# Optimization experiments

Measured on AMD Instinct MI355X. Metric: run time of the kernel, lower is better.

The kernel has to match this reference:

```python
import jax, jax.numpy as jnp
import numpy as np

EPS = 1e-5

def _lin(x, w, b):
    return x @ w + b

def _ln(x, scale, bias):
    m = jnp.mean(x, axis=-1, keepdims=True)
    v = jnp.var(x, axis=-1, keepdims=True)
    return (x - m) / jnp.sqrt(v + EPS) * scale + bias

def setup_inputs() -> dict:
    key = jax.random.key(0)
    B, N, F, OUT, TRI = 4, 128, 128, 128, 8
    ks = iter(jax.random.split(key, 64))
    def lin_params(fan_in, fan_out):
        s = 1.0 / np.sqrt(fan_in)
        w = jax.random.uniform(next(ks), (fan_in, fan_out), minval=-s, maxval=s, dtype=jnp.float32)
        b = jax.random.uniform(next(ks), (fan_out,), minval=-s, maxval=s, dtype=jnp.float32)
        return w, b
    inp = {}
    inp['node_fts'] = jax.random.normal(next(ks), (B, N, F), dtype=jnp.float32)
    inp['edge_fts'] = jax.random.normal(next(ks), (B, N, N, F), dtype=jnp.float32)
    inp['graph_fts'] = jax.random.normal(next(ks), (B, F), dtype=jnp.float32)
    inp['hidden'] = jax.random.normal(next(ks), (B, N, F), dtype=jnp.float32)
    inp['adj_matrix'] = jax.random.randint(next(ks), (B, N, N), 0, 2, dtype=jnp.int32)
    inp['m1_w'], inp['m1_b'] = lin_params(2 * F, OUT)
    inp['m2_w'], inp['m2_b'] = lin_params(2 * F, OUT)
    inp['me_w'], inp['me_b'] = lin_params(F, OUT)
    inp['mg_w'], inp['mg_b'] = lin_params(F, OUT)
    inp['mlp1_w'], inp['mlp1_b'] = lin_params(OUT, OUT)
    inp['mlp2_w'], inp['mlp2_b'] = lin_params(OUT, OUT)
    inp['o1_w'], inp['o1_b'] = lin_params(2 * F, OUT)
    inp['o2_w'], inp['o2_b'] = lin_params(OUT, OUT)
    inp['t1_w'], inp['t1_b'] = lin_params(2 * F, TRI)
    inp['t2_w'], inp['t2_b'] = lin_params(2 * F, TRI)
    inp['te1_w'], inp['te1_b'] = lin_params(F, TRI)
    inp['te2_w'], inp['te2_b'] = lin_params(F, TRI)
    inp['te3_w'], inp['te3_b'] = lin_params(F, TRI)
    inp['tg_w'], inp['tg_b'] = lin_params(F, TRI)
    inp['o3_w'], inp['o3_b'] = lin_params(TRI, OUT)
    inp['norm_scale'] = jnp.ones((OUT,), dtype=jnp.float32)
    inp['norm_bias'] = jnp.zeros((OUT,), dtype=jnp.float32)
    return inp

def reference(node_fts, edge_fts, graph_fts, hidden, adj_matrix,
              m1_w, m1_b, m2_w, m2_b, me_w, me_b, mg_w, mg_b,
              mlp1_w, mlp1_b, mlp2_w, mlp2_b,
              o1_w, o1_b, o2_w, o2_b,
              t1_w, t1_b, t2_w, t2_b,
              te1_w, te1_b, te2_w, te2_b, te3_w, te3_b,
              tg_w, tg_b, o3_w, o3_b, norm_scale, norm_bias):
    z = jnp.concatenate([node_fts, hidden], axis=-1)          # [B,N,2F]
    msg_1 = _lin(z, m1_w, m1_b)                                # [B,N,H]
    msg_2 = _lin(z, m2_w, m2_b)
    msg_e = _lin(edge_fts, me_w, me_b)                         # [B,N,N,H]
    msg_g = _lin(graph_fts, mg_w, mg_b)                        # [B,H]
    msgs = msg_1[:, None, :, :] + msg_2[:, :, None, :] + msg_e + msg_g[:, None, None, :]
    # msg_mlp: ReLU -> Linear -> ReLU -> Linear
    msgs = _lin(jax.nn.relu(_lin(jax.nn.relu(msgs), mlp1_w, mlp1_b)), mlp2_w, mlp2_b)
    # triplet messages (note: original code reuses t_1 for tri_3 -- faithful)
    tri_1 = _lin(z, t1_w, t1_b)                                # [B,N,T]
    tri_2 = _lin(z, t2_w, t2_b)
    tri_3 = _lin(z, t1_w, t1_b)
    tri_e_1 = _lin(edge_fts, te1_w, te1_b)                     # [B,N,N,T]
    tri_e_2 = _lin(edge_fts, te2_w, te2_b)
    tri_e_3 = _lin(edge_fts, te3_w, te3_b)
    tri_g = _lin(graph_fts, tg_w, tg_b)                        # [B,T]
    triplets = (tri_1[:, :, None, None, :] + tri_2[:, None, :, None, :]
                + tri_3[:, None, None, :, :]
                + tri_e_1[:, :, :, None, :] + tri_e_2[:, :, None, :, :]
                + tri_e_3[:, None, :, :, :]
                + tri_g[:, None, None, None, :])               # [B,N,N,N,T]
    tri_msgs = _lin(jnp.max(triplets, axis=1), o3_w, o3_b)     # [B,N,N,OUT]
    tri_msgs = _ln(jax.nn.relu(tri_msgs), norm_scale, norm_bias)
    # masked max aggregation
    maxarg = jnp.where(adj_matrix[..., None] == 1, msgs, -1e9)
    msgs_agg = jnp.max(maxarg, axis=1)                         # [B,N,H]
    out = jax.nn.relu(_lin(z, o1_w, o1_b) + _lin(msgs_agg, o2_w, o2_b))
    out = _ln(out, norm_scale, norm_bias)
    return out, tri_msgs
```

## Files before the change

### kernel.cpp

```cpp
#include <hip/hip_runtime.h>
#include <hip/hip_bf16.h>
#include <cstddef>
#include <cstdint>

typedef __attribute__((ext_vector_type(8))) short bf16x8;
typedef __attribute__((ext_vector_type(4))) float f32x4;
typedef unsigned short ushort_t;

__device__ __forceinline__ ushort_t f2b(float f) {
    uint32_t x = __float_as_uint(f);
    uint32_t r = (x + 0x7FFFu + ((x >> 16) & 1u)) >> 16;
    return (ushort_t)r;
}
__device__ __forceinline__ float b2f(ushort_t u) {
    return __uint_as_float(((uint32_t)u) << 16);
}

__global__ void prep_kernel(const float* __restrict__ m1_w, const float* __restrict__ m2_w,
                            const float* __restrict__ o1_w, const float* __restrict__ t1_w,
                            const float* __restrict__ t2_w,
                            const float* __restrict__ me_w, const float* __restrict__ mlp1_w,
                            const float* __restrict__ mlp2_w,
                            const float* __restrict__ te1_w, const float* __restrict__ te2_w,
                            const float* __restrict__ te3_w,
                            const float* __restrict__ graph_fts,
                            const float* __restrict__ mg_w, const float* __restrict__ mg_b,
                            const float* __restrict__ m1_b,
                            const float* __restrict__ tg_w, const float* __restrict__ t2_b,
                            const float* __restrict__ tg_b,
                            ushort_t* __restrict__ Wnt,
                            ushort_t* __restrict__ Wme, ushort_t* __restrict__ Wm1,
                            ushort_t* __restrict__ Wm2, ushort_t* __restrict__ TEt,
                            float* __restrict__ G1, float* __restrict__ TG) {
    int idx = blockIdx.x * 256 + threadIdx.x;
    if (idx < 106496) {
        int o = idx >> 8, k = idx & 255;
        float v = 0.0f;
        if (o < 128)       v = m1_w[k * 128 + o];
        else if (o < 256)  v = m2_w[k * 128 + (o - 128)];
        else if (o < 384)  v = o1_w[k * 128 + (o - 256)];
        else if (o < 392)  v = t1_w[k * 8 + (o - 384)];
        else if (o < 400)  v = t2_w[k * 8 + (o - 392)];
        Wnt[idx] = f2b(v);
    } else if (idx < 122880) {
        int t = idx - 106496, o = t >> 7, h = t & 127;
        Wme[t] = f2b(me_w[h * 128 + o]);
    } else if (idx < 139264) {
        int t = idx - 122880, o = t >> 7, h = t & 127;
        Wm1[t] = f2b(mlp1_w[h * 128 + o]);
    } else if (idx < 155648) {
        int t = idx - 139264, o = t >> 7, h = t & 127;
        Wm2[t] = f2b(mlp2_w[h * 128 + o]);
    } else if (idx < 159744) {
        int t = idx - 155648, c = t >> 7, h = t & 127;
        float v = 0.0f;
        if (c < 8)       v = te1_w[h * 8 + c];
        else if (c < 16) v = te2_w[h * 8 + (c - 8)];
        else if (c < 24) v = te3_w[h * 8 + (c - 16)];
        TEt[t] = f2b(v);
    } else if (idx < 160256) {
        int t = idx - 159744, b = t >> 7, h = t & 127;
        float a = m1_b[h] + mg_b[h];
        #pragma unroll 4
        for (int k = 0; k < 128; k++) a = fmaf(graph_fts[b * 128 + k], mg_w[k * 128 + h], a);
        G1[t] = a;
    } else if (idx < 160288) {
        int t = idx - 160256, b = t >> 3, tt = t & 7;
        float a = t2_b[tt] + tg_b[tt];
        #pragma unroll 4
        for (int k = 0; k < 128; k++) a = fmaf(graph_fts[b * 128 + k], tg_w[k * 8 + tt], a);
        TG[t] = a;
    }
}

__global__ __launch_bounds__(256)
void node_gemm(const float* __restrict__ node_fts, const float* __restrict__ hidden,
               const ushort_t* __restrict__ Wnt,
               const float* __restrict__ G1, const float* __restrict__ m2_b,
               const float* __restrict__ o1_b, const float* __restrict__ t1_b,
               const float* __restrict__ TG,
               float* __restrict__ M1, float* __restrict__ M2, float* __restrict__ O1z,
               float* __restrict__ T1v, float* __restrict__ TT2) {
    __shared__ ushort_t Zs[32 * 256];
    char* Zb = (char*)Zs;
    const int tid = threadIdx.x;
    const int blk = blockIdx.x;
    const int b = blk >> 2, q = blk & 3;
    const int row0 = b * 128 + q * 32;
    const int w = tid >> 6, l = tid & 63, g = l >> 4, lq = l & 15;

    const float4* nsrc = reinterpret_cast<const float4*>(node_fts + (size_t)row0 * 128);
    const float4* hsrc = reinterpret_cast<const float4*>(hidden + (size_t)row0 * 128);
    #pragma unroll
    for (int p = 0; p < 8; p++) {
        int idx = tid + p * 256;
        int r = idx >> 6, c4 = idx & 63;
        float4 v = (c4 < 32) ? nsrc[r * 32 + c4] : hsrc[r * 32 + (c4 - 32)];
        uint2 pk;
        pk.x = (uint32_t)f2b(v.x) | ((uint32_t)f2b(v.y) << 16);
        pk.y = (uint32_t)f2b(v.z) | ((uint32_t)f2b(v.w) << 16);
        *reinterpret_cast<uint2*>(Zb + r * 512 + (((c4 >> 1) ^ (r & 7)) << 4) + (c4 & 1) * 8) = pk;
    }
    __syncthreads();

    for (int mt = w; mt < 26; mt += 4) {
        f32x4 acc0 = (f32x4){0.f, 0.f, 0.f, 0.f};
        f32x4 acc1 = (f32x4){0.f, 0.f, 0.f, 0.f};
        const ushort_t* arow = Wnt + (size_t)(mt * 16 + lq) * 256;
        #pragma unroll
        for (int ks = 0; ks < 8; ks++) {
            bf16x8 a = *reinterpret_cast<const bf16x8*>(arow + ks * 32 + g * 8);
            int j0 = lq, j1 = 16 + lq;
            bf16x8 b0 = *reinterpret_cast<const bf16x8*>(Zb + j0 * 512 + (((ks * 4 + g) ^ (j0 & 7)) << 4));
            bf16x8 b1 = *reinterpret_cast<const bf16x8*>(Zb + j1 * 512 + (((ks * 4 + g) ^ (j1 & 7)) << 4));
            acc0 = __builtin_amdgcn_mfma_f32_16x16x32_bf16(a, b0, acc0, 0, 0, 0);
            acc1 = __builtin_amdgcn_mfma_f32_16x16x32_bf16(a, b1, acc1, 0, 0, 0);
        }
        #pragma unroll
        for (int half = 0; half < 2; half++) {
            const f32x4 acc = half ? acc1 : acc0;
            const int grow = row0 + half * 16 + lq;
            #pragma unroll
            for (int c = 0; c < 4; c++) {
                int o = mt * 16 + g * 4 + c;
                float v = acc[c];
                if (o < 128)       M1[(size_t)grow * 128 + o] = v + G1[b * 128 + o];
                else if (o < 256)  M2[(size_t)grow * 128 + (o - 128)] = v + m2_b[o - 128];
                else if (o < 384)  O1z[(size_t)grow * 128 + (o - 256)] = v + o1_b[o - 256];
                else if (o < 392)  T1v[(size_t)grow * 8 + (o - 384)] = v + t1_b[o - 384];
                else if (o < 400)  TT2[(size_t)grow * 8 + (o - 392)] = v + TG[b * 8 + (o - 392)];
            }
        }
    }
}

__device__ __forceinline__ void mm128(const ushort_t* __restrict__ Wt, const char* Xb,
                                      f32x4 acc[4][4], int o_blk, int j_blk, int g, int lq) {
    #pragma unroll
    for (int ks = 0; ks < 4; ks++) {
        bf16x8 a[4], bb[4];
        #pragma unroll
        for (int m = 0; m < 4; m++)
            a[m] = *reinterpret_cast<const bf16x8*>(Wt + (size_t)(o_blk + m * 16 + lq) * 128 + ks * 32 + g * 8);
        #pragma unroll
        for (int n = 0; n < 4; n++) {
            int j = j_blk + n * 16 + lq;
            bb[n] = *reinterpret_cast<const bf16x8*>(Xb + j * 256 + (((ks * 4 + g) ^ (j & 7)) << 4));
        }
        #pragma unroll
        for (int m = 0; m < 4; m++)
            #pragma unroll
            for (int n = 0; n < 4; n++)
                acc[m][n] = __builtin_amdgcn_mfma_f32_16x16x32_bf16(a[m], bb[n], acc[m][n], 0, 0, 0);
    }
}

__global__ __launch_bounds__(256, 2)
void edge_kernel(const float* __restrict__ edge_fts,
                 const ushort_t* __restrict__ Wme, const float* __restrict__ me_b,
                 const ushort_t* __restrict__ Wm1, const float* __restrict__ mlp1_b,
                 const ushort_t* __restrict__ Wm2, const float* __restrict__ mlp2_b,
                 const ushort_t* __restrict__ TEt,
                 const float* __restrict__ te1_b, const float* __restrict__ te2_b,
                 const float* __restrict__ te3_b,
                 const float* __restrict__ M1,  const float* __restrict__ M2,
                 const float* __restrict__ T1v, const float* __restrict__ TT2,
                 ushort_t* __restrict__ msgsM, float* __restrict__ T1buf,
                 float* __restrict__ T2buf, float* __restrict__ E3buf) {
    __shared__ ushort_t Xs[16384];
    char* Xb = (char*)Xs;
    const int tid = threadIdx.x;
    const int b  = blockIdx.x >> 7;
    const int ie = blockIdx.x & 127;
    const int w = tid >> 6, l = tid & 63, g = l >> 4, lq = l & 15;
    const int o_blk = (w & 1) * 64, j_blk = (w >> 1) * 64;

    const float4* esrc = reinterpret_cast<const float4*>(edge_fts + (size_t)(b * 128 + ie) * 16384);
    #pragma unroll
    for (int p = 0; p < 16; p++) {
        int idx = tid + p * 256;
        int r = idx >> 5, c4 = idx & 31;
        float4 v = esrc[idx];
        uint2 pk;
        pk.x = (uint32_t)f2b(v.x) | ((uint32_t)f2b(v.y) << 16);
        pk.y = (uint32_t)f2b(v.z) | ((uint32_t)f2b(v.w) << 16);
        *reinterpret_cast<uint2*>(Xb + r * 256 + (((c4 >> 1) ^ (r & 7)) << 4) + (c4 & 1) * 8) = pk;
    }
    __syncthreads();

    {
        const int m_te = w & 1;
        const ushort_t* At = TEt + m_te * 16 * 128;
        f32x4 acc[4];
        #pragma unroll
        for (int n = 0; n < 4; n++) acc[n] = (f32x4){0.f, 0.f, 0.f, 0.f};
        #pragma unroll
        for (int ks = 0; ks < 4; ks++) {
            bf16x8 a = *reinterpret_cast<const bf16x8*>(At + lq * 128 + ks * 32 + g * 8);
            #pragma unroll
            for (int n = 0; n < 4; n++) {
                int j = j_blk + n * 16 + lq;
                bf16x8 bbv = *reinterpret_cast<const bf16x8*>(Xb + j * 256 + (((ks * 4 + g) ^ (j & 7)) << 4));
                acc[n] = __builtin_amdgcn_mfma_f32_16x16x32_bf16(a, bbv, acc[n], 0, 0, 0);
            }
        }
        if (m_te == 0) {
            if (g < 2) {
                int t0 = g * 4;
                const float4 eb = *reinterpret_cast<const float4*>(te1_b + t0);
                const float4 tv = *reinterpret_cast<const float4*>(T1v + (size_t)(b * 128 + ie) * 8 + t0);
                #pragma unroll
                for (int n = 0; n < 4; n++) {
                    int j = j_blk + n * 16 + lq;
                    float4 o4 = make_float4(acc[n][0] + eb.x + tv.x, acc[n][1] + eb.y + tv.y,
                                            acc[n][2] + eb.z + tv.z, acc[n][3] + eb.w + tv.w);
                    *reinterpret_cast<float4*>(T1buf + ((size_t)(b * 128 + j) * 128 + ie) * 8 + t0) = o4;
                }
            } else {
                int t0 = g * 4 - 8;
                const float4 eb = *reinterpret_cast<const float4*>(te2_b + t0);
                #pragma unroll
                for (int n = 0; n < 4; n++) {
                    int j = j_blk + n * 16 + lq;
                    float4 o4 = make_float4(acc[n][0] + eb.x, acc[n][1] + eb.y,
                                            acc[n][2] + eb.z, acc[n][3] + eb.w);
                    *reinterpret_cast<float4*>(T2buf + ((size_t)(b * 128 + ie) * 128 + j) * 8 + t0) = o4;
                }
            }
        } else if (g < 2) {
            int t0 = g * 4;
            const float4 eb = *reinterpret_cast<const float4*>(te3_b + t0);
            const float4 t2v = *reinterpret_cast<const float4*>(TT2 + (size_t)(b * 128 + ie) * 8 + t0);
            #pragma unroll
            for (int n = 0; n < 4; n++) {
                int j = j_blk + n * 16 + lq;
                const float4 t3v = *reinterpret_cast<const float4*>(T1v + (size_t)(b * 128 + j) * 8 + t0);
                float4 o4 = make_float4(acc[n][0] + eb.x + t2v.x + t3v.x,
                                        acc[n][1] + eb.y + t2v.y + t3v.y,
                                        acc[n][2] + eb.z + t2v.z + t3v.z,
                                        acc[n][3] + eb.w + t2v.w + t3v.w);
                *reinterpret_cast<float4*>(E3buf + ((size_t)(b * 128 + ie) * 128 + j) * 8 + t0) = o4;
            }
        }
    }

    f32x4 acc[4][4];

    #pragma unroll
    for (int m = 0; m < 4; m++)
        #pragma unroll
        for (int n = 0; n < 4; n++) acc[m][n] = (f32x4){0.f, 0.f, 0.f, 0.f};
    mm128(Wme, Xb, acc, o_blk, j_blk, g, lq);
    {
        float4 bc[4];
        #pragma unroll
        for (int m = 0; m < 4; m++) {
            int o0 = o_blk + m * 16 + g * 4;
            const float4 eb = *reinterpret_cast<const float4*>(me_b + o0);
            const float4 m2 = *reinterpret_cast<const float4*>(M2 + (size_t)(b * 128 + ie) * 128 + o0);
            bc[m] = make_float4(eb.x + m2.x, eb.y + m2.y, eb.z + m2.z, eb.w + m2.w);
        }
        __syncthreads();
        #pragma unroll
        for (int m = 0; m < 4; m++) {
            int o0 = o_blk + m * 16 + g * 4;
            #pragma unroll
            for (int n = 0; n < 4; n++) {
                int j = j_blk + n * 16 + lq;
                const float4 m1 = *reinterpret_cast<const float4*>(M1 + (size_t)(b * 128 + j) * 128 + o0);
                float r0 = fmaxf(acc[m][n][0] + bc[m].x + m1.x, 0.f);
                float r1 = fmaxf(acc[m][n][1] + bc[m].y + m1.y, 0.f);
                float r2 = fmaxf(acc[m][n][2] + bc[m].z + m1.z, 0.f);
                float r3 = fmaxf(acc[m][n][3] + bc[m].w + m1.w, 0.f);
                uint2 pk;
                pk.x = (uint32_t)f2b(r0) | ((uint32_t)f2b(r1) << 16);
                pk.y = (uint32_t)f2b(r2) | ((uint32_t)f2b(r3) << 16);
                *reinterpret_cast<uint2*>(Xb + j * 256 + ((((o0 >> 3) ^ (j & 7))) << 4) + (o0 & 7) * 2) = pk;
            }
        }
        __syncthreads();
    }

    #pragma unroll
    for (int m = 0; m < 4; m++)
        #pragma unroll
        for (int n = 0; n < 4; n++) acc[m][n] = (f32x4){0.f, 0.f, 0.f, 0.f};
    mm128(Wm1, Xb, acc, o_blk, j_blk, g, lq);
    {
        float4 bc[4];
        #pragma unroll
        for (int m = 0; m < 4; m++) {
            int o0 = o_blk + m * 16 + g * 4;
            bc[m] = *reinterpret_cast<const float4*>(mlp1_b + o0);
        }
        __syncthreads();
        #pragma unroll
        for (int m = 0; m < 4; m++) {
            int o0 = o_blk + m * 16 + g * 4;
            #pragma unroll
            for (int n = 0; n < 4; n++) {
                int j = j_blk + n * 16 + lq;
                float r0 = fmaxf(acc[m][n][0] + bc[m].x, 0.f);
                float r1 = fmaxf(acc[m][n][1] + bc[m].y, 0.f);
                float r2 = fmaxf(acc[m][n][2] + bc[m].z, 0.f);
                float r3 = fmaxf(acc[m][n][3] + bc[m].w, 0.f);
                uint2 pk;
                pk.x = (uint32_t)f2b(r0) | ((uint32_t)f2b(r1) << 16);
                pk.y = (uint32_t)f2b(r2) | ((uint32_t)f2b(r3) << 16);
                *reinterpret_cast<uint2*>(Xb + j * 256 + ((((o0 >> 3) ^ (j & 7))) << 4) + (o0 & 7) * 2) = pk;
            }
        }
        __syncthreads();
    }

    #pragma unroll
    for (int m = 0; m < 4; m++)
        #pragma unroll
        for (int n = 0; n < 4; n++) acc[m][n] = (f32x4){0.f, 0.f, 0.f, 0.f};
    mm128(Wm2, Xb, acc, o_blk, j_blk, g, lq);
    {
        float4 bc[4];
        #pragma unroll
        for (int m = 0; m < 4; m++) {
            int o0 = o_blk + m * 16 + g * 4;
            bc[m] = *reinterpret_cast<const float4*>(mlp2_b + o0);
        }
        __syncthreads();
        #pragma unroll
        for (int m = 0; m < 4; m++) {
            int o0 = o_blk + m * 16 + g * 4;
            #pragma unroll
            for (int n = 0; n < 4; n++) {
                int j = j_blk + n * 16 + lq;
                float r0 = acc[m][n][0] + bc[m].x;
                float r1 = acc[m][n][1] + bc[m].y;
                float r2 = acc[m][n][2] + bc[m].z;
                float r3 = acc[m][n][3] + bc[m].w;
                uint2 pk;
                pk.x = (uint32_t)f2b(r0) | ((uint32_t)f2b(r1) << 16);
                pk.y = (uint32_t)f2b(r2) | ((uint32_t)f2b(r3) << 16);
                *reinterpret_cast<uint2*>(Xb + j * 256 + ((((o0 >> 3) ^ (j & 7))) << 4) + (o0 & 7) * 2) = pk;
            }
        }
        __syncthreads();
    }

    {
        const int r0 = tid >> 4, sc = tid & 15;
        #pragma unroll
        for (int q = 0; q < 8; q++) {
            int r = r0 + q * 16;
            uint4 v = *reinterpret_cast<const uint4*>(Xb + r * 256 + sc * 16);
            int logical = sc ^ (r & 7);
            *reinterpret_cast<uint4*>(msgsM + ((size_t)(b * 128 + r) * 128 + ie) * 128 + logical * 8) = v;
        }
    }
}

__global__ __launch_bounds__(256)
void agg_out_kernel(const ushort_t* __restrict__ msgsM, const int* __restrict__ adj,
                    const float* __restrict__ O1z,
                    const float* __restrict__ o2_w, const float* __restrict__ o2_b,
                    const float* __restrict__ scale, const float* __restrict__ bias,
                    float* __restrict__ out) {
    __shared__ float aggs[4][128];
    __shared__ float fagg[128];
    __shared__ float red[2][2];
    const int b = blockIdx.x >> 7, j = blockIdx.x & 127;
    const int t = threadIdx.x;
    const int wv = t >> 6, ln = t & 63;
    const ushort_t* msrc = msgsM + (size_t)(b * 128 + j) * 16384;
    const int* arow = adj + b * 16384 + j;
    float a0 = -1e9f, a1 = -1e9f;
    #pragma unroll 8
    for (int s = 0; s < 32; s++) {
        const int i = s * 4 + wv;
        uint32_t u = *reinterpret_cast<const uint32_t*>(msrc + i * 128 + ln * 2);
        bool m = (arow[i * 128] == 1);
        float x0 = b2f((ushort_t)(u & 0xffffu));
        float x1 = b2f((ushort_t)(u >> 16));
        a0 = m ? fmaxf(a0, x0) : a0;
        a1 = m ? fmaxf(a1, x1) : a1;
    }
    aggs[wv][ln * 2]     = a0;
    aggs[wv][ln * 2 + 1] = a1;
    __syncthreads();
    if (t < 128)
        fagg[t] = fmaxf(fmaxf(aggs[0][t], aggs[1][t]), fmaxf(aggs[2][t], aggs[3][t]));
    __syncthreads();

    float v = 0.0f;
    if (t < 128) {
        float val = o2_b[t] + O1z[(size_t)(b * 128 + j) * 128 + t];
        #pragma unroll 4
        for (int k = 0; k < 128; k++) val = fmaf(fagg[k], o2_w[k * 128 + t], val);
        v = fmaxf(val, 0.0f);
    }
    float s = v, s2 = v * v;
    #pragma unroll
    for (int off = 32; off >= 1; off >>= 1) {
        s += __shfl_down(s, off, 64);
        s2 += __shfl_down(s2, off, 64);
    }
    if (t < 128 && (t & 63) == 0) { red[t >> 6][0] = s; red[t >> 6][1] = s2; }
    __syncthreads();
    if (t < 128) {
        const float tot = red[0][0] + red[1][0];
        const float tot2 = red[0][1] + red[1][1];
        const float mean = tot * (1.0f / 128.0f);
        const float var = tot2 * (1.0f / 128.0f) - mean * mean;
        const float rstd = rsqrtf(var + 1e-5f);
        out[(size_t)(b * 128 + j) * 128 + t] = (v - mean) * rstd * scale[t] + bias[t];
    }
}

__global__ __launch_bounds__(512)
void tri_kernel(const float* __restrict__ T1buf, const float* __restrict__ T2buf,
                const float* __restrict__ E3buf, const float* __restrict__ o3_w,
                const float* __restrict__ o3_b, const float* __restrict__ scale,
                const float* __restrict__ bias, float* __restrict__ tri_out) {
    __shared__ __align__(16) float T1s[1024];
    __shared__ __align__(16) float E3s[1024];
    __shared__ __align__(16) float o3s[1024];
    __shared__ __align__(16) float Ps[4][128][8];
    const int b = blockIdx.x >> 7, jf = blockIdx.x & 127;
    const int tid = threadIdx.x;
    if (tid < 256) {
        reinterpret_cast<float4*>(T1s)[tid] =
            reinterpret_cast<const float4*>(T1buf + (size_t)(b * 128 + jf) * 1024)[tid];
        reinterpret_cast<float4*>(o3s)[tid] = reinterpret_cast<const float4*>(o3_w)[tid];
    } else {
        int t2 = tid - 256;
        reinterpret_cast<float4*>(E3s)[t2] =
            reinterpret_cast<const float4*>(E3buf + (size_t)(b * 128 + jf) * 1024)[t2];
    }
    __syncthreads();

    {
        const int kf = tid & 127, ih = tid >> 7;
        float a8[8];
        #pragma unroll
        for (int t = 0; t < 8; t++) a8[t] = -3.0e38f;
        const float4* t2p = reinterpret_cast<const float4*>(T2buf + (size_t)b * 131072);
        #pragma unroll 4
        for (int ii = 0; ii < 32; ++ii) {
            const int i = ih * 32 + ii;
            const float4 p = t2p[(i * 128 + kf) * 2];
            const float4 q = t2p[(i * 128 + kf) * 2 + 1];
            const float* t1r = &T1s[i * 8];
            a8[0] = fmaxf(a8[0], t1r[0] + p.x);
            a8[1] = fmaxf(a8[1], t1r[1] + p.y);
            a8[2] = fmaxf(a8[2], t1r[2] + p.z);
            a8[3] = fmaxf(a8[3], t1r[3] + p.w);
            a8[4] = fmaxf(a8[4], t1r[4] + q.x);
            a8[5] = fmaxf(a8[5], t1r[5] + q.y);
            a8[6] = fmaxf(a8[6], t1r[6] + q.z);
            a8[7] = fmaxf(a8[7], t1r[7] + q.w);
        }
        #pragma unroll
        for (int t = 0; t < 8; t++) Ps[ih][kf][t] = a8[t];
    }
    __syncthreads();

    const int w = tid >> 6, l = tid & 63;
    const float ob0 = o3_b[l],     ob1 = o3_b[l + 64];
    const float sc0 = scale[l],    sc1 = scale[l + 64];
    const float bi0 = bias[l],     bi1 = bias[l + 64];
    for (int kk = 0; kk < 16; ++kk) {
        const int kf = w * 16 + kk;
        float m8[8];
        #pragma unroll
        for (int t = 0; t < 8; t++)
            m8[t] = fmaxf(fmaxf(Ps[0][kf][t], Ps[1][kf][t]),
                          fmaxf(Ps[2][kf][t], Ps[3][kf][t])) + E3s[kf * 8 + t];
        float v0 = ob0, v1 = ob1;
        #pragma unroll
        for (int t = 0; t < 8; t++) {
            v0 = fmaf(m8[t], o3s[t * 128 + l], v0);
            v1 = fmaf(m8[t], o3s[t * 128 + l + 64], v1);
        }
        v0 = fmaxf(v0, 0.0f);
        v1 = fmaxf(v1, 0.0f);
        float s = v0 + v1, s2 = v0 * v0 + v1 * v1;
        #pragma unroll
        for (int off = 32; off >= 1; off >>= 1) {
            s  += __shfl_xor(s, off, 64);
            s2 += __shfl_xor(s2, off, 64);
        }
        const float mean = s * (1.0f / 128.0f);
        const float var = s2 * (1.0f / 128.0f) - mean * mean;
        const float rstd = rsqrtf(var + 1e-5f);
        float* dst = tri_out + (size_t)((b * 128 + jf) * 128 + kf) * 128;
        dst[l]      = (v0 - mean) * rstd * sc0 + bi0;
        dst[l + 64] = (v1 - mean) * rstd * sc1 + bi1;
    }
}

extern "C" void kernel_launch(void* const* d_in, const int* in_sizes, int n_in,
                              void* d_out, int out_size, void* d_ws, size_t ws_size,
                              hipStream_t stream) {
    const float* node_fts  = (const float*)d_in[0];
    const float* edge_fts  = (const float*)d_in[1];
    const float* graph_fts = (const float*)d_in[2];
    const float* hidden    = (const float*)d_in[3];
    const int*   adj       = (const int*)d_in[4];
    const float* m1_w = (const float*)d_in[5],  *m1_b = (const float*)d_in[6];
    const float* m2_w = (const float*)d_in[7],  *m2_b = (const float*)d_in[8];
    const float* me_w = (const float*)d_in[9],  *me_b = (const float*)d_in[10];
    const float* mg_w = (const float*)d_in[11], *mg_b = (const float*)d_in[12];
    const float* mlp1_w = (const float*)d_in[13], *mlp1_b = (const float*)d_in[14];
    const float* mlp2_w = (const float*)d_in[15], *mlp2_b = (const float*)d_in[16];
    const float* o1_w = (const float*)d_in[17], *o1_b = (const float*)d_in[18];
    const float* o2_w = (const float*)d_in[19], *o2_b = (const float*)d_in[20];
    const float* t1_w = (const float*)d_in[21], *t1_b = (const float*)d_in[22];
    const float* t2_w = (const float*)d_in[23], *t2_b = (const float*)d_in[24];
    const float* te1_w = (const float*)d_in[25], *te1_b = (const float*)d_in[26];
    const float* te2_w = (const float*)d_in[27], *te2_b = (const float*)d_in[28];
    const float* te3_w = (const float*)d_in[29], *te3_b = (const float*)d_in[30];
    const float* tg_w = (const float*)d_in[31], *tg_b = (const float*)d_in[32];
    const float* o3_w = (const float*)d_in[33], *o3_b = (const float*)d_in[34];
    const float* norm_scale = (const float*)d_in[35];
    const float* norm_bias  = (const float*)d_in[36];

    char* w8 = (char*)d_ws;
    float*    M1    = (float*)(w8 + 0);
    float*    M2    = (float*)(w8 + 262144);
    float*    O1z   = (float*)(w8 + 524288);
    float*    T1v   = (float*)(w8 + 786432);
    float*    TT2   = (float*)(w8 + 802816);
    ushort_t* Wme   = (ushort_t*)(w8 + 819200);
    ushort_t* Wm1   = (ushort_t*)(w8 + 851968);
    ushort_t* Wm2   = (ushort_t*)(w8 + 884736);
    ushort_t* TEt   = (ushort_t*)(w8 + 917504);
    ushort_t* msgsM = (ushort_t*)(w8 + 925696);
    float*    T1buf = (float*)(w8 + 17702912);
    float*    T2buf = (float*)(w8 + 19800064);
    float*    E3buf = (float*)(w8 + 21897216);
    ushort_t* Wnt   = (ushort_t*)(w8 + 23994368);
    float*    G1    = (float*)(w8 + 24207360);
    float*    TG    = (float*)(w8 + 24209408);

    float* out_p  = (float*)d_out;
    float* tri_p  = (float*)d_out + 65536;

    prep_kernel<<<627, 256, 0, stream>>>(m1_w, m2_w, o1_w, t1_w, t2_w,
                                         me_w, mlp1_w, mlp2_w, te1_w, te2_w, te3_w,
                                         graph_fts, mg_w, mg_b, m1_b, tg_w, t2_b, tg_b,
                                         Wnt, Wme, Wm1, Wm2, TEt, G1, TG);
    node_gemm<<<16, 256, 0, stream>>>(node_fts, hidden, Wnt, G1, m2_b, o1_b, t1_b, TG,
                                      M1, M2, O1z, T1v, TT2);
    edge_kernel<<<512, 256, 0, stream>>>(edge_fts, Wme, me_b, Wm1, mlp1_b, Wm2, mlp2_b,
                                         TEt, te1_b, te2_b, te3_b,
                                         M1, M2, T1v, TT2, msgsM, T1buf, T2buf, E3buf);
    agg_out_kernel<<<512, 256, 0, stream>>>(msgsM, adj, O1z, o2_w, o2_b,
                                            norm_scale, norm_bias, out_p);
    tri_kernel<<<512, 512, 0, stream>>>(T1buf, T2buf, E3buf, o3_w, o3_b,
                                        norm_scale, norm_bias, tri_p);
}
```

Baseline: 111.3 us.

## Split edge kernel rows across two blocks with ping-pong LDS buffers

The edge kernel now handles 64 of the 128 j-rows per block, doubling the grid to 1024 blocks and raising the launch-bounds occupancy hint from 2 to 4. Shared memory is split into two 16 KB buffers used alternately across the three chained GEMMs, which removes the barrier that previously sat before each in-place write-back. Manual bf16 rounding is replaced by the packed __float22bfloat162_rn conversion. The goal is better CU occupancy and latency hiding, at the cost of each block reloading the weight tiles for half as much work.

```diff
diff --git a/kernel.cpp b/kernel.cpp
--- a/kernel.cpp
+++ b/kernel.cpp
@@ -2,6 +2,7 @@
 #include <hip/hip_bf16.h>
 #include <cstddef>
 #include <cstdint>
+#include <cstring>
 
 typedef __attribute__((ext_vector_type(8))) short bf16x8;
 typedef __attribute__((ext_vector_type(4))) float f32x4;
@@ -14,6 +15,12 @@
 }
 __device__ __forceinline__ float b2f(ushort_t u) {
     return __uint_as_float(((uint32_t)u) << 16);
+}
+__device__ __forceinline__ uint32_t pk2(float x, float y) {
+    __hip_bfloat162 h = __float22bfloat162_rn(float2{x, y});
+    uint32_t u;
+    __builtin_memcpy(&u, &h, 4);
+    return u;
 }
 
 __global__ void prep_kernel(const float* __restrict__ m1_w, const float* __restrict__ m2_w,
@@ -97,8 +104,8 @@
         int r = idx >> 6, c4 = idx & 63;
         float4 v = (c4 < 32) ? nsrc[r * 32 + c4] : hsrc[r * 32 + (c4 - 32)];
         uint2 pk;
-        pk.x = (uint32_t)f2b(v.x) | ((uint32_t)f2b(v.y) << 16);
-        pk.y = (uint32_t)f2b(v.z) | ((uint32_t)f2b(v.w) << 16);
+        pk.x = pk2(v.x, v.y);
+        pk.y = pk2(v.z, v.w);
         *reinterpret_cast<uint2*>(Zb + r * 512 + (((c4 >> 1) ^ (r & 7)) << 4) + (c4 & 1) * 8) = pk;
     }
     __syncthreads();
@@ -134,28 +141,28 @@
     }
 }
 
-__device__ __forceinline__ void mm128(const ushort_t* __restrict__ Wt, const char* Xb,
-                                      f32x4 acc[4][4], int o_blk, int j_blk, int g, int lq) {
+__device__ __forceinline__ void mm64(const ushort_t* __restrict__ Wt, const char* Xa,
+                                     f32x4 acc[4][2], int o_blk, int j_blk, int g, int lq) {
     #pragma unroll
     for (int ks = 0; ks < 4; ks++) {
-        bf16x8 a[4], bb[4];
+        bf16x8 a[4], bb[2];
         #pragma unroll
         for (int m = 0; m < 4; m++)
             a[m] = *reinterpret_cast<const bf16x8*>(Wt + (size_t)(o_blk + m * 16 + lq) * 128 + ks * 32 + g * 8);
         #pragma unroll
-        for (int n = 0; n < 4; n++) {
+        for (int n = 0; n < 2; n++) {
             int j = j_blk + n * 16 + lq;
-            bb[n] = *reinterpret_cast<const bf16x8*>(Xb + j * 256 + (((ks * 4 + g) ^ (j & 7)) << 4));
+            bb[n] = *reinterpret_cast<const bf16x8*>(Xa + j * 256 + (((ks * 4 + g) ^ (j & 7)) << 4));
         }
         #pragma unroll
         for (int m = 0; m < 4; m++)
             #pragma unroll
-            for (int n = 0; n < 4; n++)
+            for (int n = 0; n < 2; n++)
                 acc[m][n] = __builtin_amdgcn_mfma_f32_16x16x32_bf16(a[m], bb[n], acc[m][n], 0, 0, 0);
     }
 }
 
-__global__ __launch_bounds__(256, 2)
+__global__ __launch_bounds__(256, 4)
 void edge_kernel(const float* __restrict__ edge_fts,
                  const ushort_t* __restrict__ Wme, const float* __restrict__ me_b,
                  const ushort_t* __restrict__ Wm1, const float* __restrict__ mlp1_b,
@@ -167,41 +174,44 @@
                  const float* __restrict__ T1v, const float* __restrict__ TT2,
                  ushort_t* __restrict__ msgsM, float* __restrict__ T1buf,
                  float* __restrict__ T2buf, float* __restrict__ E3buf) {
-    __shared__ ushort_t Xs[16384];
-    char* Xb = (char*)Xs;
+    __shared__ ushort_t Xs[2][8192];
+    char* X0 = (char*)Xs[0];
+    char* X1 = (char*)Xs[1];
     const int tid = threadIdx.x;
-    const int b  = blockIdx.x >> 7;
-    const int ie = blockIdx.x & 127;
+    const int b  = blockIdx.x >> 8;
+    const int ie = (blockIdx.x >> 1) & 127;
+    const int jrow0 = (blockIdx.x & 1) * 64;
     const int w = tid >> 6, l = tid & 63, g = l >> 4, lq = l & 15;
-    const int o_blk = (w & 1) * 64, j_blk = (w >> 1) * 64;
-
-    const float4* esrc = reinterpret_cast<const float4*>(edge_fts + (size_t)(b * 128 + ie) * 16384);
-    #pragma unroll
-    for (int p = 0; p < 16; p++) {
+    const int o_blk = (w & 1) * 64, j_blk = (w >> 1) * 32;
+
+    const float4* esrc = reinterpret_cast<const float4*>(
+        edge_fts + ((size_t)(b * 128 + ie) * 128 + jrow0) * 128);
+    #pragma unroll
+    for (int p = 0; p < 8; p++) {
         int idx = tid + p * 256;
         int r = idx >> 5, c4 = idx & 31;
         float4 v = esrc[idx];
         uint2 pk;
-        pk.x = (uint32_t)f2b(v.x) | ((uint32_t)f2b(v.y) << 16);
-        pk.y = (uint32_t)f2b(v.z) | ((uint32_t)f2b(v.w) << 16);
-        *reinterpret_cast<uint2*>(Xb + r * 256 + (((c4 >> 1) ^ (r & 7)) << 4) + (c4 & 1) * 8) = pk;
+        pk.x = pk2(v.x, v.y);
+        pk.y = pk2(v.z, v.w);
+        *reinterpret_cast<uint2*>(X0 + r * 256 + (((c4 >> 1) ^ (r & 7)) << 4) + (c4 & 1) * 8) = pk;
     }
     __syncthreads();
 
     {
         const int m_te = w & 1;
         const ushort_t* At = TEt + m_te * 16 * 128;
-        f32x4 acc[4];
-        #pragma unroll
-        for (int n = 0; n < 4; n++) acc[n] = (f32x4){0.f, 0.f, 0.f, 0.f};
+        f32x4 acc2[2];
+        #pragma unroll
+        for (int n = 0; n < 2; n++) acc2[n] = (f32x4){0.f, 0.f, 0.f, 0.f};
         #pragma unroll
         for (int ks = 0; ks < 4; ks++) {
             bf16x8 a = *reinterpret_cast<const bf16x8*>(At + lq * 128 + ks * 32 + g * 8);
             #pragma unroll
-            for (int n = 0; n < 4; n++) {
+            for (int n = 0; n < 2; n++) {
                 int j = j_blk + n * 16 + lq;
-                bf16x8 bbv = *reinterpret_cast<const bf16x8*>(Xb + j * 256 + (((ks * 4 + g) ^ (j & 7)) << 4));
-                acc[n] = __builtin_amdgcn_mfma_f32_16x16x32_bf16(a, bbv, acc[n], 0, 0, 0);
+                bf16x8 bbv = *reinterpret_cast<const bf16x8*>(X0 + j * 256 + (((ks * 4 + g) ^ (j & 7)) << 4));
+                acc2[n] = __builtin_amdgcn_mfma_f32_16x16x32_bf16(a, bbv, acc2[n], 0, 0, 0);
             }
         }
         if (m_te == 0) {
@@ -210,21 +220,21 @@
                 const float4 eb = *reinterpret_cast<const float4*>(te1_b + t0);
                 const float4 tv = *reinterpret_cast<const float4*>(T1v + (size_t)(b * 128 + ie) * 8 + t0);
                 #pragma unroll
-                for (int n = 0; n < 4; n++) {
-                    int j = j_blk + n * 16 + lq;
-                    float4 o4 = make_float4(acc[n][0] + eb.x + tv.x, acc[n][1] + eb.y + tv.y,
-                                            acc[n][2] + eb.z + tv.z, acc[n][3] + eb.w + tv.w);
-                    *reinterpret_cast<float4*>(T1buf + ((size_t)(b * 128 + j) * 128 + ie) * 8 + t0) = o4;
+                for (int n = 0; n < 2; n++) {
+                    int jg = jrow0 + j_blk + n * 16 + lq;
+                    float4 o4 = make_float4(acc2[n][0] + eb.x + tv.x, acc2[n][1] + eb.y + tv.y,
+                                            acc2[n][2] + eb.z + tv.z, acc2[n][3] + eb.w + tv.w);
+                    *reinterpret_cast<float4*>(T1buf + ((size_t)(b * 128 + jg) * 128 + ie) * 8 + t0) = o4;
                 }
             } else {
                 int t0 = g * 4 - 8;
                 const float4 eb = *reinterpret_cast<const float4*>(te2_b + t0);
                 #pragma unroll
-                for (int n = 0; n < 4; n++) {
-                    int j = j_blk + n * 16 + lq;
-                    float4 o4 = make_float4(acc[n][0] + eb.x, acc[n][1] + eb.y,
-                                            acc[n][2] + eb.z, acc[n][3] + eb.w);
-                    *reinterpret_cast<float4*>(T2buf + ((size_t)(b * 128 + ie) * 128 + j) * 8 + t0) = o4;
+                for (int n = 0; n < 2; n++) {
+                    int jg = jrow0 + j_blk + n * 16 + lq;
+                    float4 o4 = make_float4(acc2[n][0] + eb.x, acc2[n][1] + eb.y,
+                                            acc2[n][2] + eb.z, acc2[n][3] + eb.w);
+                    *reinterpret_cast<float4*>(T2buf + ((size_t)(b * 128 + ie) * 128 + jg) * 8 + t0) = o4;
                 }
             }
         } else if (g < 2) {
@@ -232,25 +242,25 @@
             const float4 eb = *reinterpret_cast<const float4*>(te3_b + t0);
             const float4 t2v = *reinterpret_cast<const float4*>(TT2 + (size_t)(b * 128 + ie) * 8 + t0);
             #pragma unroll
-            for (int n = 0; n < 4; n++) {
-                int j = j_blk + n * 16 + lq;
-                const float4 t3v = *reinterpret_cast<const float4*>(T1v + (size_t)(b * 128 + j) * 8 + t0);
-                float4 o4 = make_float4(acc[n][0] + eb.x + t2v.x + t3v.x,
-                                        acc[n][1] + eb.y + t2v.y + t3v.y,
-                                        acc[n][2] + eb.z + t2v.z + t3v.z,
-                                        acc[n][3] + eb.w + t2v.w + t3v.w);
-                *reinterpret_cast<float4*>(E3buf + ((size_t)(b * 128 + ie) * 128 + j) * 8 + t0) = o4;
-            }
-        }
-    }
-
-    f32x4 acc[4][4];
+            for (int n = 0; n < 2; n++) {
+                int jg = jrow0 + j_blk + n * 16 + lq;
+                const float4 t3v = *reinterpret_cast<const float4*>(T1v + (size_t)(b * 128 + jg) * 8 + t0);
+                float4 o4 = make_float4(acc2[n][0] + eb.x + t2v.x + t3v.x,
+                                        acc2[n][1] + eb.y + t2v.y + t3v.y,
+                                        acc2[n][2] + eb.z + t2v.z + t3v.z,
+                                        acc2[n][3] + eb.w + t2v.w + t3v.w);
+                *reinterpret_cast<float4*>(E3buf + ((size_t)(b * 128 + ie) * 128 + jg) * 8 + t0) = o4;
+            }
+        }
+    }
+
+    f32x4 acc[4][2];
 
     #pragma unroll
     for (int m = 0; m < 4; m++)
         #pragma unroll
-        for (int n = 0; n < 4; n++) acc[m][n] = (f32x4){0.f, 0.f, 0.f, 0.f};
-    mm128(Wme, Xb, acc, o_blk, j_blk, g, lq);
+        for (int n = 0; n < 2; n++) acc[m][n] = (f32x4){0.f, 0.f, 0.f, 0.f};
+    mm64(Wme, X0, acc, o_blk, j_blk, g, lq);
     {
         float4 bc[4];
         #pragma unroll
@@ -260,22 +270,22 @@
             const float4 m2 = *reinterpret_cast<const float4*>(M2 + (size_t)(b * 128 + ie) * 128 + o0);
             bc[m] = make_float4(eb.x + m2.x, eb.y + m2.y, eb.z + m2.z, eb.w + m2.w);
         }
-        __syncthreads();
         #pragma unroll
         for (int m = 0; m < 4; m++) {
             int o0 = o_blk + m * 16 + g * 4;
             #pragma unroll
-            for (int n = 0; n < 4; n++) {
+            for (int n = 0; n < 2; n++) {
                 int j = j_blk + n * 16 + lq;
-                const float4 m1 = *reinterpret_cast<const float4*>(M1 + (size_t)(b * 128 + j) * 128 + o0);
+                int jg = jrow0 + j;
+                const float4 m1 = *reinterpret_cast<const float4*>(M1 + (size_t)(b * 128 + jg) * 128 + o0);
                 float r0 = fmaxf(acc[m][n][0] + bc[m].x + m1.x, 0.f);
                 float r1 = fmaxf(acc[m][n][1] + bc[m].y + m1.y, 0.f);
                 float r2 = fmaxf(acc[m][n][2] + bc[m].z + m1.z, 0.f);
                 float r3 = fmaxf(acc[m][n][3] + bc[m].w + m1.w, 0.f);
                 uint2 pk;
-                pk.x = (uint32_t)f2b(r0) | ((uint32_t)f2b(r1) << 16);
-                pk.y = (uint32_t)f2b(r2) | ((uint32_t)f2b(r3) << 16);
-                *reinterpret_cast<uint2*>(Xb + j * 256 + ((((o0 >> 3) ^ (j & 7))) << 4) + (o0 & 7) * 2) = pk;
+                pk.x = pk2(r0, r1);
+                pk.y = pk2(r2, r3);
+                *reinterpret_cast<uint2*>(X1 + j * 256 + ((((o0 >> 3) ^ (j & 7))) << 4) + (o0 & 7) * 2) = pk;
             }
         }
         __syncthreads();
@@ -284,62 +294,50 @@
     #pragma unroll
     for (int m = 0; m < 4; m++)
         #pragma unroll
-        for (int n = 0; n < 4; n++) acc[m][n] = (f32x4){0.f, 0.f, 0.f, 0.f};
-    mm128(Wm1, Xb, acc, o_blk, j_blk, g, lq);
+        for (int n = 0; n < 2; n++) acc[m][n] = (f32x4){0.f, 0.f, 0.f, 0.f};
+    mm64(Wm1, X1, acc, o_blk, j_blk, g, lq);
     {
-        float4 bc[4];
         #pragma unroll
         for (int m = 0; m < 4; m++) {
             int o0 = o_blk + m * 16 + g * 4;
-            bc[m] = *reinterpret_cast<const float4*>(mlp1_b + o0);
+            const float4 bb = *reinterpret_cast<const float4*>(mlp1_b + o0);
+            #pragma unroll
+            for (int n = 0; n < 2; n++) {
+                int j = j_blk + n * 16 + lq;
+                float r0 = fmaxf(acc[m][n][0] + bb.x, 0.f);
+                float r1 = fmaxf(acc[m][n][1] + bb.y, 0.f);
+                float r2 = fmaxf(acc[m][n][2] + bb.z, 0.f);
+                float r3 = fmaxf(acc[m][n][3] + bb.w, 0.f);
+                uint2 pk;
+                pk.x = pk2(r0, r1);
+                pk.y = pk2(r2, r3);
+                *reinterpret_cast<uint2*>(X0 + j * 256 + ((((o0 >> 3) ^ (j & 7))) << 4) + (o0 & 7) * 2) = pk;
+            }
         }
         __syncthreads();
+    }
+
+    #pragma unroll
+    for (int m = 0; m < 4; m++)
+        #pragma unroll
+        for (int n = 0; n < 2; n++) acc[m][n] = (f32x4){0.f, 0.f, 0.f, 0.f};
+    mm64(Wm2, X0, acc, o_blk, j_blk, g, lq);
+    {
         #pragma unroll
         for (int m = 0; m < 4; m++) {
             int o0 = o_blk + m * 16 + g * 4;
-            #pragma unroll
-            for (int n = 0; n < 4; n++) {
+            const float4 bb = *reinterpret_cast<const float4*>(mlp2_b + o0);
+            #pragma unroll
+            for (int n = 0; n < 2; n++) {
                 int j = j_blk + n * 16 + lq;
-                float r0 = fmaxf(acc[m][n][0] + bc[m].x, 0.f);
-                float r1 = fmaxf(acc[m][n][1] + bc[m].y, 0.f);
-                float r2 = fmaxf(acc[m][n][2] + bc[m].z, 0.f);
-                float r3 = fmaxf(acc[m][n][3] + bc[m].w, 0.f);
+                float r0 = acc[m][n][0] + bb.x;
+                float r1 = acc[m][n][1] + bb.y;
+                float r2 = acc[m][n][2] + bb.z;
+                float r3 = acc[m][n][3] + bb.w;
                 uint2 pk;
-                pk.x = (uint32_t)f2b(r0) | ((uint32_t)f2b(r1) << 16);
-                pk.y = (uint32_t)f2b(r2) | ((uint32_t)f2b(r3) << 16);
-                *reinterpret_cast<uint2*>(Xb + j * 256 + ((((o0 >> 3) ^ (j & 7))) << 4) + (o0 & 7) * 2) = pk;
-            }
-        }
-        __syncthreads();
-    }
-
-    #pragma unroll
-    for (int m = 0; m < 4; m++)
-        #pragma unroll
-        for (int n = 0; n < 4; n++) acc[m][n] = (f32x4){0.f, 0.f, 0.f, 0.f};
-    mm128(Wm2, Xb, acc, o_blk, j_blk, g, lq);
-    {
-        float4 bc[4];
-        #pragma unroll
-        for (int m = 0; m < 4; m++) {
-            int o0 = o_blk + m * 16 + g * 4;
-            bc[m] = *reinterpret_cast<const float4*>(mlp2_b + o0);
-        }
-        __syncthreads();
-        #pragma unroll
-        for (int m = 0; m < 4; m++) {
-            int o0 = o_blk + m * 16 + g * 4;
-            #pragma unroll
-            for (int n = 0; n < 4; n++) {
-                int j = j_blk + n * 16 + lq;
-                float r0 = acc[m][n][0] + bc[m].x;
-                float r1 = acc[m][n][1] + bc[m].y;
-                float r2 = acc[m][n][2] + bc[m].z;
-                float r3 = acc[m][n][3] + bc[m].w;
-                uint2 pk;
-                pk.x = (uint32_t)f2b(r0) | ((uint32_t)f2b(r1) << 16);
-                pk.y = (uint32_t)f2b(r2) | ((uint32_t)f2b(r3) << 16);
-                *reinterpret_cast<uint2*>(Xb + j * 256 + ((((o0 >> 3) ^ (j & 7))) << 4) + (o0 & 7) * 2) = pk;
+                pk.x = pk2(r0, r1);
+                pk.y = pk2(r2, r3);
+                *reinterpret_cast<uint2*>(X1 + j * 256 + ((((o0 >> 3) ^ (j & 7))) << 4) + (o0 & 7) * 2) = pk;
             }
         }
         __syncthreads();
@@ -348,11 +346,11 @@
     {
         const int r0 = tid >> 4, sc = tid & 15;
         #pragma unroll
-        for (int q = 0; q < 8; q++) {
+        for (int q = 0; q < 4; q++) {
             int r = r0 + q * 16;
-            uint4 v = *reinterpret_cast<const uint4*>(Xb + r * 256 + sc * 16);
+            uint4 v = *reinterpret_cast<const uint4*>(X1 + r * 256 + sc * 16);
             int logical = sc ^ (r & 7);
-            *reinterpret_cast<uint4*>(msgsM + ((size_t)(b * 128 + r) * 128 + ie) * 128 + logical * 8) = v;
+            *reinterpret_cast<uint4*>(msgsM + ((size_t)(b * 128 + jrow0 + r) * 128 + ie) * 128 + logical * 8) = v;
         }
     }
 }
@@ -549,9 +547,9 @@
                                          Wnt, Wme, Wm1, Wm2, TEt, G1, TG);
     node_gemm<<<16, 256, 0, stream>>>(node_fts, hidden, Wnt, G1, m2_b, o1_b, t1_b, TG,
                                       M1, M2, O1z, T1v, TT2);
-    edge_kernel<<<512, 256, 0, stream>>>(edge_fts, Wme, me_b, Wm1, mlp1_b, Wm2, mlp2_b,
-                                         TEt, te1_b, te2_b, te3_b,
-                                         M1, M2, T1v, TT2, msgsM, T1buf, T2buf, E3buf);
+    edge_kernel<<<1024, 256, 0, stream>>>(edge_fts, Wme, me_b, Wm1, mlp1_b, Wm2, mlp2_b,
+                                          TEt, te1_b, te2_b, te3_b,
+                                          M1, M2, T1v, TT2, msgsM, T1buf, T2buf, E3buf);
     agg_out_kernel<<<512, 256, 0, stream>>>(msgsM, adj, O1z, o2_w, o2_b,
                                             norm_scale, norm_bias, out_p);
     tri_kernel<<<512, 512, 0, stream>>>(T1buf, T2buf, E3buf, o3_w, o3_b,
```

Result: slower. 119.9 us (+7.7%).
